# Kernel tuning notes

Measured on AMD Instinct MI355X. Metric: run time of the kernel, lower is better.

## Reference

```python
import jax, jax.numpy as jnp
import numpy as np

B, C, D, H, W = 2, 128, 32, 64, 64  # ch_in=128, shurink=0 -> Cs = ch_out = C
Cs = C


def setup_inputs() -> dict:
    key = jax.random.key(0)
    ks = jax.random.split(key, 9)
    std = 1.0 / np.sqrt(C).astype(np.float32)
    x = jax.random.normal(ks[0], (B, C, D, H, W), jnp.float32)
    Wk = jax.random.normal(ks[1], (Cs, C), jnp.float32) * std
    bk = jax.random.normal(ks[2], (Cs,), jnp.float32) * std
    Wq = jax.random.normal(ks[3], (Cs, C), jnp.float32) * std
    bq = jax.random.normal(ks[4], (Cs,), jnp.float32) * std
    Wv = jax.random.normal(ks[5], (Cs, C), jnp.float32) * std
    bv = jax.random.normal(ks[6], (Cs,), jnp.float32) * std
    Wo = jax.random.normal(ks[7], (C, Cs), jnp.float32) * (1.0 / np.sqrt(Cs).astype(np.float32))
    bo = jax.random.normal(ks[8], (C,), jnp.float32) * std
    return {"x": x, "Wk": Wk, "bk": bk, "Wq": Wq, "bq": bq, "Wv": Wv, "bv": bv, "Wo": Wo, "bo": bo}


def reference(x, Wk, bk, Wq, bq, Wv, bv, Wo, bo):
    # 1x1x1 Conv3d == per-voxel linear over channels
    def proj(Wt, bt):
        return jnp.einsum('bcdhw,oc->bodhw', x, Wt) + bt[None, :, None, None, None]

    K = proj(Wk, bk)  # [B,Cs,D,H,W]
    Q = proj(Wq, bq)
    V = proj(Wv, bv)

    scale = 1.0 / jnp.sqrt(jnp.asarray(Cs, x.dtype))
    # per-pixel depth attention: scores[b,h,w,i,j] = sum_c K[b,c,i,h,w] * Q[b,c,j,h,w]
    scores = jnp.einsum('bcihw,bcjhw->bhwij', K, Q) * scale
    # torch softmax dim=1 on [N,D,D] == key-position axis i (axis=-2 here)
    A = jax.nn.softmax(scores, axis=-2)
    # a[b,c,j,h,w] = sum_i V[b,c,i,h,w] * A[b,h,w,i,j]  (== bmm(V, A))
    a = jnp.einsum('bcihw,bhwij->bcjhw', V, A)
    out = jnp.einsum('bcjhw,oc->bojhw', a, Wo) + bo[None, :, None, None, None]
    return x + out  # atten_factor = 1
```

## Files before the change

### kernel.cpp

```cpp
#include <hip/hip_runtime.h>

typedef _Float16 f16x8 __attribute__((ext_vector_type(8)));
typedef _Float16 f16x4 __attribute__((ext_vector_type(4)));
typedef float    f32x4 __attribute__((ext_vector_type(4)));

#define MFMA(a,b,c) __builtin_amdgcn_mfma_f32_16x16x32_f16((a),(b),(c),0,0,0)


__global__ __launch_bounds__(128) void prep_kernel(
    const float* __restrict__ Wk, const float* __restrict__ bk,
    const float* __restrict__ Wq, const float* __restrict__ bq,
    const float* __restrict__ Wv, const float* __restrict__ bv,
    const float* __restrict__ Wo, const float* __restrict__ bo,
    _Float16* __restrict__ wh, float* __restrict__ bf) {
  __shared__ float worow[128];
  const int o = blockIdx.x;
  const int c = threadIdx.x;
  const float scale = 0.08838834764831844f;
  worow[c] = Wo[o*128 + c];
  __syncthreads();
  float acc = 0.f, a2 = 0.f;
  for (int m = 0; m < 128; ++m) {
    acc += worow[m] * Wv[m*128 + c];
    a2  += worow[m] * bv[m];
  }
  wh[o*128+c]         = (_Float16)(Wk[o*128+c] * scale);
  wh[16384 + o*128+c] = (_Float16)(Wq[o*128+c]);
  wh[32768 + o*128+c] = (_Float16)acc;
  if (c == 0) {
    bf[o]       = bk[o] * scale;
    bf[128 + o] = bq[o];
    bf[256 + o] = a2 + bo[o];
  }
}

__global__ __launch_bounds__(256) void transpose_kernel(
    const float* __restrict__ x, _Float16* __restrict__ Xg) {
  __shared__ _Float16 Lt[64 * 130];
  const int bid = blockIdx.x;
  const int h = bid & 63, d = (bid >> 6) & 31, b = bid >> 11;
  const int tid = threadIdx.x;
  const size_t rbase = (size_t)b*16777216u + (size_t)d*4096 + h*64;
#pragma unroll
  for (int i = 0; i < 8; ++i) {
    const int chunk = tid + i*256;
    const int c = chunk >> 4, wq = chunk & 15;
    const f32x4 v = *(const f32x4*)(x + rbase + (size_t)c*131072 + wq*4);
    Lt[(wq*4+0)*130 + c] = (_Float16)v[0];
    Lt[(wq*4+1)*130 + c] = (_Float16)v[1];
    Lt[(wq*4+2)*130 + c] = (_Float16)v[2];
    Lt[(wq*4+3)*130 + c] = (_Float16)v[3];
  }
  __syncthreads();
  const int gbase = b*1024 + h*16;
#pragma unroll
  for (int i = 0; i < 4; ++i) {
    const int idx = tid + i*256;
    const int w = idx >> 4, ck = (idx & 15) * 8;
    const int wg = w >> 2, p = w & 3;
    const f16x8 v = *(const f16x8*)(Lt + w*130 + ck);
    *(f16x8*)(Xg + (size_t)(gbase + wg)*16384 + (p*32 + d)*128 + ck) = v;
  }
}

__device__ __forceinline__ f16x4 cvt4(f32x4 v, f32x4 b) {
  f16x4 r;
  r[0] = (_Float16)(v[0] + b[0]); r[1] = (_Float16)(v[1] + b[1]);
  r[2] = (_Float16)(v[2] + b[2]); r[3] = (_Float16)(v[3] + b[3]);
  return r;
}
__device__ __forceinline__ f16x4 cvt4z(f32x4 v) {
  f16x4 r;
  r[0] = (_Float16)v[0]; r[1] = (_Float16)v[1];
  r[2] = (_Float16)v[2]; r[3] = (_Float16)v[3];
  return r;
}

__global__ __launch_bounds__(1024) void attn_kernel(
    const _Float16* __restrict__ Xg, const _Float16* __restrict__ wh,
    const float* __restrict__ bfp, float* __restrict__ out) {
  __shared__ __align__(16) char lds[133120];
  _Float16* Xt = (_Float16*)(lds);
  _Float16* Kt = (_Float16*)(lds + 34816);
  _Float16* Qt = (_Float16*)(lds + 69632);
  float*    Sm = (float*)(lds + 104448);
  _Float16* At = (_Float16*)(lds + 122880);
  float*    ot = (float*)(lds + 34816);

  const int tid  = threadIdx.x;
  const int lane = tid & 63;
  const int wv   = tid >> 6;
  const int quad = lane >> 4;
  const int l15  = lane & 15;
  const int mi   = wv & 7;
  const int ni   = wv >> 3;

  const int bid = blockIdx.x;
  const int g = (bid & ~31) | ((bid & 7) << 2) | ((bid >> 3) & 3);
  const int b   = g >> 10;
  const int rem = g & 1023;
  const int h   = rem >> 4;
  const int wg  = rem & 15;
  const size_t pbase = (size_t)b * 16777216u + (size_t)(h*64 + wg*4);

  f16x8 wk[4], wq[4], wp[4];
  {
    const int wrow = (mi*16 + l15) * 128;
#pragma unroll
    for (int kk = 0; kk < 4; ++kk) {
      const int off = wrow + kk*32 + quad*8;
      wk[kk] = *(const f16x8*)(wh + off);
      wq[kk] = *(const f16x8*)(wh + 16384 + off);
      wp[kk] = *(const f16x8*)(wh + 32768 + off);
    }
  }
  const f32x4 bk4 = *(const f32x4*)(bfp +       mi*16 + quad*4);
  const f32x4 bq4 = *(const f32x4*)(bfp + 128 + mi*16 + quad*4);
  const f32x4 bp4 = *(const f32x4*)(bfp + 256 + mi*16 + quad*4);
  const f32x4 zz = {0.f, 0.f, 0.f, 0.f};

  {
    const _Float16* src = Xg + (size_t)g * 16384;
#pragma unroll
    for (int i = 0; i < 2; ++i) {
      const int idx = tid + i*1024;
      const int row = idx >> 4, ck = (idx & 15) * 8;
      const f16x8 v = *(const f16x8*)(src + row*128 + ck);
      *(f16x8*)(Xt + row*136 + ck) = v;
    }
  }
  __syncthreads();

  {
    f32x4 aK[4] = {zz, zz, zz, zz};
    f32x4 aQ[4] = {zz, zz, zz, zz};
#pragma unroll
    for (int kk = 0; kk < 4; ++kk) {
      const int co = kk*32 + quad*8;
      f16x8 bfv[4];
#pragma unroll
      for (int nt = 0; nt < 4; ++nt)
        bfv[nt] = *(const f16x8*)(Xt + (ni*64 + nt*16 + l15)*136 + co);
#pragma unroll
      for (int nt = 0; nt < 4; ++nt) {
        aK[nt] = MFMA(wk[kk], bfv[nt], aK[nt]);
        aQ[nt] = MFMA(wq[kk], bfv[nt], aQ[nt]);
      }
    }
#pragma unroll
    for (int nt = 0; nt < 4; ++nt) {
      const int ad = (ni*64 + nt*16 + l15)*136 + mi*16 + quad*4;
      *(f16x4*)(Kt + ad) = cvt4(aK[nt], bk4);
      *(f16x4*)(Qt + ad) = cvt4(aQ[nt], bq4);
    }
  }
  __syncthreads();

  {
    const int p = wv >> 2, ti = (wv >> 1) & 1, tj = wv & 1;
    f32x4 aS = zz;
#pragma unroll
    for (int kk = 0; kk < 4; ++kk) {
      const int co = kk*32 + quad*8;
      const f16x8 ak  = *(const f16x8*)(Kt + (p*32 + ti*16 + l15)*136 + co);
      const f16x8 bq_ = *(const f16x8*)(Qt + (p*32 + tj*16 + l15)*136 + co);
      aS = MFMA(ak, bq_, aS);
    }
    *(f32x4*)(Sm + (p*32 + tj*16 + l15)*36 + ti*16 + quad*4) = aS;
  }
  __syncthreads();

  if (tid < 128) {
    const float* srow = Sm + tid*36;
    float mx = srow[0];
#pragma unroll
    for (int i = 1; i < 32; ++i) mx = fmaxf(mx, srow[i]);
    float den = 0.f;
#pragma unroll
    for (int i = 0; i < 32; ++i) den += __expf(srow[i] - mx);
    const float rr = 1.0f / den;
    _Float16* arow = At + tid*40;
#pragma unroll
    for (int i = 0; i < 32; ++i) arow[i] = (_Float16)(__expf(srow[i] - mx) * rr);
  }
  __syncthreads();

  {
    const int p = wv & 3, mg = wv >> 2;
    f16x8 bA[2];
#pragma unroll
    for (int tj = 0; tj < 2; ++tj)
      bA[tj] = *(const f16x8*)(At + (p*32 + tj*16 + l15)*40 + quad*8);
#pragma unroll
    for (int t2 = 0; t2 < 2; ++t2) {
      const int ms = mg*2 + t2;
      const int cbase = (p*32 + quad*8)*136 + ms*16 + l15;
      const f16x8 ax = { Xt[cbase], Xt[cbase+136], Xt[cbase+272], Xt[cbase+408],
                         Xt[cbase+544], Xt[cbase+680], Xt[cbase+816], Xt[cbase+952] };
#pragma unroll
      for (int tj = 0; tj < 2; ++tj) {
        f32x4 aU = MFMA(ax, bA[tj], zz);
        *(f16x4*)(Kt + (p*32 + tj*16 + l15)*136 + ms*16 + quad*4) = cvt4z(aU);
      }
    }
  }
  __syncthreads();

  f32x4 aO[4] = {zz, zz, zz, zz};
#pragma unroll
  for (int kk = 0; kk < 4; ++kk) {
    const int co = kk*32 + quad*8;
    f16x8 bfv[4];
#pragma unroll
    for (int nt = 0; nt < 4; ++nt)
      bfv[nt] = *(const f16x8*)(Kt + (ni*64 + nt*16 + l15)*136 + co);
#pragma unroll
    for (int nt = 0; nt < 4; ++nt)
      aO[nt] = MFMA(wp[kk], bfv[nt], aO[nt]);
  }
  __syncthreads();

#pragma unroll
  for (int nt = 0; nt < 4; ++nt) {
    const int col = ni*64 + nt*16 + l15;
    const int pp = col >> 5, jj = col & 31;
    float* dst = ot + (mi*16 + quad*4)*132 + jj*4 + pp;
    dst[0]   = aO[nt][0] + bp4[0];
    dst[132] = aO[nt][1] + bp4[1];
    dst[264] = aO[nt][2] + bp4[2];
    dst[396] = aO[nt][3] + bp4[3];
  }
  __syncthreads();

#pragma unroll
  for (int it = 0; it < 4; ++it) {
    const int o = it*32 + (tid >> 5);
    const int j = tid & 31;
    f32x4 v = *(const f32x4*)(ot + o*132 + j*4);
    v[0] += (float)Xt[(0*32 + j)*136 + o];
    v[1] += (float)Xt[(1*32 + j)*136 + o];
    v[2] += (float)Xt[(2*32 + j)*136 + o];
    v[3] += (float)Xt[(3*32 + j)*136 + o];
    *(f32x4*)(out + pbase + (size_t)o*131072 + j*4096) = v;
  }
}

extern "C" void kernel_launch(void* const* d_in, const int* in_sizes, int n_in,
                              void* d_out, int out_size, void* d_ws, size_t ws_size,
                              hipStream_t stream) {
  const float* x  = (const float*)d_in[0];
  const float* Wk = (const float*)d_in[1];
  const float* bk = (const float*)d_in[2];
  const float* Wq = (const float*)d_in[3];
  const float* bq = (const float*)d_in[4];
  const float* Wv = (const float*)d_in[5];
  const float* bv = (const float*)d_in[6];
  const float* Wo = (const float*)d_in[7];
  const float* bo = (const float*)d_in[8];
  float* out = (float*)d_out;
  _Float16* wh = (_Float16*)d_ws;
  float* bf = (float*)((char*)d_ws + 98304);
  _Float16* Xg = (_Float16*)((char*)d_ws + 131072);

  prep_kernel<<<dim3(128), dim3(128), 0, stream>>>(Wk, bk, Wq, bq, Wv, bv, Wo, bo, wh, bf);
  transpose_kernel<<<dim3(4096), dim3(256), 0, stream>>>(x, Xg);
  attn_kernel<<<dim3(2048), dim3(1024), 0, stream>>>(Xg, wh, bf, out);
}
```

Measured before the change: 378.7 us.

## Fold Wk·Wq into one projection, fuse transpose into attention kernel

Precomputes M = Wk^T·Wq (scaled) so scores become X^T·(M X + t), which removes one of the two projection GEMMs. The separate fp32-to-fp16 transpose kernel and its workspace round trip are dropped: the attention kernel now reads x directly into XOR-swizzled LDS. Softmax is computed in registers with wave shuffles, so the score staging buffer and one barrier go away. LDS usage drops, which could allow more resident blocks; the cost is uncoalesced strided global loads of x and possible fp16 precision loss from the folded weight product.

```diff
diff --git a/kernel.cpp b/kernel.cpp
--- a/kernel.cpp
+++ b/kernel.cpp
@@ -13,54 +13,23 @@
     const float* __restrict__ Wv, const float* __restrict__ bv,
     const float* __restrict__ Wo, const float* __restrict__ bo,
     _Float16* __restrict__ wh, float* __restrict__ bf) {
-  __shared__ float worow[128];
+  __shared__ float shK[128], shO[128];
   const int o = blockIdx.x;
   const int c = threadIdx.x;
   const float scale = 0.08838834764831844f;
-  worow[c] = Wo[o*128 + c];
-  __syncthreads();
-  float acc = 0.f, a2 = 0.f;
+  shK[c] = Wk[c*128 + o];
+  shO[c] = Wo[o*128 + c];
+  __syncthreads();
+  float aM = 0.f, aV = 0.f, tK = 0.f, bV = 0.f;
   for (int m = 0; m < 128; ++m) {
-    acc += worow[m] * Wv[m*128 + c];
-    a2  += worow[m] * bv[m];
-  }
-  wh[o*128+c]         = (_Float16)(Wk[o*128+c] * scale);
-  wh[16384 + o*128+c] = (_Float16)(Wq[o*128+c]);
-  wh[32768 + o*128+c] = (_Float16)acc;
-  if (c == 0) {
-    bf[o]       = bk[o] * scale;
-    bf[128 + o] = bq[o];
-    bf[256 + o] = a2 + bo[o];
-  }
-}
-
-__global__ __launch_bounds__(256) void transpose_kernel(
-    const float* __restrict__ x, _Float16* __restrict__ Xg) {
-  __shared__ _Float16 Lt[64 * 130];
-  const int bid = blockIdx.x;
-  const int h = bid & 63, d = (bid >> 6) & 31, b = bid >> 11;
-  const int tid = threadIdx.x;
-  const size_t rbase = (size_t)b*16777216u + (size_t)d*4096 + h*64;
-#pragma unroll
-  for (int i = 0; i < 8; ++i) {
-    const int chunk = tid + i*256;
-    const int c = chunk >> 4, wq = chunk & 15;
-    const f32x4 v = *(const f32x4*)(x + rbase + (size_t)c*131072 + wq*4);
-    Lt[(wq*4+0)*130 + c] = (_Float16)v[0];
-    Lt[(wq*4+1)*130 + c] = (_Float16)v[1];
-    Lt[(wq*4+2)*130 + c] = (_Float16)v[2];
-    Lt[(wq*4+3)*130 + c] = (_Float16)v[3];
-  }
-  __syncthreads();
-  const int gbase = b*1024 + h*16;
-#pragma unroll
-  for (int i = 0; i < 4; ++i) {
-    const int idx = tid + i*256;
-    const int w = idx >> 4, ck = (idx & 15) * 8;
-    const int wg = w >> 2, p = w & 3;
-    const f16x8 v = *(const f16x8*)(Lt + w*130 + ck);
-    *(f16x8*)(Xg + (size_t)(gbase + wg)*16384 + (p*32 + d)*128 + ck) = v;
-  }
+    aM += shK[m] * Wq[m*128 + c];
+    aV += shO[m] * Wv[m*128 + c];
+    tK += shK[m] * bq[m];
+    bV += shO[m] * bv[m];
+  }
+  wh[o*128 + c]         = (_Float16)(aM * scale);
+  wh[16384 + o*128 + c] = (_Float16)aV;
+  if (c == 0) { bf[o] = tK * scale; bf[128 + o] = bV + bo[o]; }
 }
 
 __device__ __forceinline__ f16x4 cvt4(f32x4 v, f32x4 b) {
@@ -76,24 +45,23 @@
   return r;
 }
 
-__global__ __launch_bounds__(1024) void attn_kernel(
-    const _Float16* __restrict__ Xg, const _Float16* __restrict__ wh,
+__device__ __forceinline__ int xsw(int row, int col ) {
+  return ((row << 8) | (col << 1)) ^ (((row ^ (row >> 2)) & 7) << 4);
+}
+
+__global__ __launch_bounds__(1024, 8) void attn_kernel(
+    const float* __restrict__ x, const _Float16* __restrict__ wh,
     const float* __restrict__ bfp, float* __restrict__ out) {
-  __shared__ __align__(16) char lds[133120];
-  _Float16* Xt = (_Float16*)(lds);
-  _Float16* Kt = (_Float16*)(lds + 34816);
-  _Float16* Qt = (_Float16*)(lds + 69632);
-  float*    Sm = (float*)(lds + 104448);
-  _Float16* At = (_Float16*)(lds + 122880);
-  float*    ot = (float*)(lds + 34816);
+  __shared__ __align__(16) char lds[75776];
+  char* XtB = lds;
+  char* YtB = lds + 32768;
+  _Float16* At = (_Float16*)(lds + 65536);
 
   const int tid  = threadIdx.x;
   const int lane = tid & 63;
   const int wv   = tid >> 6;
   const int quad = lane >> 4;
   const int l15  = lane & 15;
-  const int mi   = wv & 7;
-  const int ni   = wv >> 3;
 
   const int bid = blockIdx.x;
   const int g = (bid & ~31) | ((bid & 7) << 2) | ((bid >> 3) & 3);
@@ -102,90 +70,98 @@
   const int h   = rem >> 4;
   const int wg  = rem & 15;
   const size_t pbase = (size_t)b * 16777216u + (size_t)(h*64 + wg*4);
-
-  f16x8 wk[4], wq[4], wp[4];
-  {
-    const int wrow = (mi*16 + l15) * 128;
-#pragma unroll
-    for (int kk = 0; kk < 4; ++kk) {
-      const int off = wrow + kk*32 + quad*8;
-      wk[kk] = *(const f16x8*)(wh + off);
-      wq[kk] = *(const f16x8*)(wh + 16384 + off);
-      wp[kk] = *(const f16x8*)(wh + 32768 + off);
-    }
-  }
-  const f32x4 bk4 = *(const f32x4*)(bfp +       mi*16 + quad*4);
-  const f32x4 bq4 = *(const f32x4*)(bfp + 128 + mi*16 + quad*4);
-  const f32x4 bp4 = *(const f32x4*)(bfp + 256 + mi*16 + quad*4);
   const f32x4 zz = {0.f, 0.f, 0.f, 0.f};
 
-  {
-    const _Float16* src = Xg + (size_t)g * 16384;
-#pragma unroll
-    for (int i = 0; i < 2; ++i) {
+  const int mi = wv & 7, ni = wv >> 3;
+  f16x8 wm[4];
+#pragma unroll
+  for (int kk = 0; kk < 4; ++kk)
+    wm[kk] = *(const f16x8*)(wh + (mi*16 + l15)*128 + kk*32 + quad*8);
+  const f32x4 t4 = *(const f32x4*)(bfp + mi*16 + quad*4);
+
+  {
+    const float* xg = x + pbase;
+#pragma unroll
+    for (int i = 0; i < 4; ++i) {
       const int idx = tid + i*1024;
-      const int row = idx >> 4, ck = (idx & 15) * 8;
-      const f16x8 v = *(const f16x8*)(src + row*128 + ck);
-      *(f16x8*)(Xt + row*136 + ck) = v;
-    }
-  }
-  __syncthreads();
-
-  {
-    f32x4 aK[4] = {zz, zz, zz, zz};
-    f32x4 aQ[4] = {zz, zz, zz, zz};
+      const int c = idx & 127, dd = idx >> 7;
+      const f32x4 v = *(const f32x4*)(xg + (size_t)c*131072 + (size_t)dd*4096);
+#pragma unroll
+      for (int p = 0; p < 4; ++p)
+        *(_Float16*)(XtB + xsw(dd*4 + p, c)) = (_Float16)v[p];
+    }
+  }
+  __syncthreads();
+
+  {
+    f32x4 aY[4] = {zz, zz, zz, zz};
 #pragma unroll
     for (int kk = 0; kk < 4; ++kk) {
       const int co = kk*32 + quad*8;
-      f16x8 bfv[4];
-#pragma unroll
-      for (int nt = 0; nt < 4; ++nt)
-        bfv[nt] = *(const f16x8*)(Xt + (ni*64 + nt*16 + l15)*136 + co);
 #pragma unroll
       for (int nt = 0; nt < 4; ++nt) {
-        aK[nt] = MFMA(wk[kk], bfv[nt], aK[nt]);
-        aQ[nt] = MFMA(wq[kk], bfv[nt], aQ[nt]);
-      }
-    }
-#pragma unroll
-    for (int nt = 0; nt < 4; ++nt) {
-      const int ad = (ni*64 + nt*16 + l15)*136 + mi*16 + quad*4;
-      *(f16x4*)(Kt + ad) = cvt4(aK[nt], bk4);
-      *(f16x4*)(Qt + ad) = cvt4(aQ[nt], bq4);
-    }
-  }
-  __syncthreads();
-
-  {
-    const int p = wv >> 2, ti = (wv >> 1) & 1, tj = wv & 1;
-    f32x4 aS = zz;
+        const f16x8 bfv = *(const f16x8*)(XtB + xsw(ni*64 + nt*16 + l15, co));
+        aY[nt] = MFMA(wm[kk], bfv, aY[nt]);
+      }
+    }
+#pragma unroll
+    for (int nt = 0; nt < 4; ++nt)
+      *(f16x4*)(YtB + xsw(ni*64 + nt*16 + l15, mi*16 + quad*4)) = cvt4(aY[nt], t4);
+  }
+  __syncthreads();
+
+  if (wv < 4) {
+    const int p = wv;
+    f32x4 aS[2][2] = {{zz, zz}, {zz, zz}};
 #pragma unroll
     for (int kk = 0; kk < 4; ++kk) {
       const int co = kk*32 + quad*8;
-      const f16x8 ak  = *(const f16x8*)(Kt + (p*32 + ti*16 + l15)*136 + co);
-      const f16x8 bq_ = *(const f16x8*)(Qt + (p*32 + tj*16 + l15)*136 + co);
-      aS = MFMA(ak, bq_, aS);
-    }
-    *(f32x4*)(Sm + (p*32 + tj*16 + l15)*36 + ti*16 + quad*4) = aS;
-  }
-  __syncthreads();
-
-  if (tid < 128) {
-    const float* srow = Sm + tid*36;
-    float mx = srow[0];
-#pragma unroll
-    for (int i = 1; i < 32; ++i) mx = fmaxf(mx, srow[i]);
-    float den = 0.f;
-#pragma unroll
-    for (int i = 0; i < 32; ++i) den += __expf(srow[i] - mx);
-    const float rr = 1.0f / den;
-    _Float16* arow = At + tid*40;
-#pragma unroll
-    for (int i = 0; i < 32; ++i) arow[i] = (_Float16)(__expf(srow[i] - mx) * rr);
-  }
-  __syncthreads();
-
-  {
+      f16x8 ak[2], by[2];
+#pragma unroll
+      for (int t = 0; t < 2; ++t) {
+        ak[t] = *(const f16x8*)(XtB + xsw((t*16 + l15)*4 + p, co));
+        by[t] = *(const f16x8*)(YtB + xsw((t*16 + l15)*4 + p, co));
+      }
+#pragma unroll
+      for (int ti = 0; ti < 2; ++ti)
+#pragma unroll
+        for (int tj = 0; tj < 2; ++tj)
+          aS[ti][tj] = MFMA(ak[ti], by[tj], aS[ti][tj]);
+    }
+#pragma unroll
+    for (int tj = 0; tj < 2; ++tj) {
+      float mx = aS[0][tj][0];
+#pragma unroll
+      for (int r = 1; r < 4; ++r) mx = fmaxf(mx, aS[0][tj][r]);
+#pragma unroll
+      for (int r = 0; r < 4; ++r) mx = fmaxf(mx, aS[1][tj][r]);
+      mx = fmaxf(mx, __shfl_xor(mx, 16));
+      mx = fmaxf(mx, __shfl_xor(mx, 32));
+      float e[2][4];
+      float den = 0.f;
+#pragma unroll
+      for (int ti = 0; ti < 2; ++ti)
+#pragma unroll
+        for (int r = 0; r < 4; ++r) { e[ti][r] = __expf(aS[ti][tj][r] - mx); den += e[ti][r]; }
+      den += __shfl_xor(den, 16);
+      den += __shfl_xor(den, 32);
+      const float rr = 1.0f / den;
+#pragma unroll
+      for (int ti = 0; ti < 2; ++ti) {
+        f16x4 av;
+#pragma unroll
+        for (int r = 0; r < 4; ++r) av[r] = (_Float16)(e[ti][r] * rr);
+        *(f16x4*)(At + (p*32 + tj*16 + l15)*40 + ti*16 + quad*4) = av;
+      }
+    }
+  }
+  __syncthreads();
+
+  f16x8 wp[4];
+  {
+#pragma unroll
+    for (int kk = 0; kk < 4; ++kk)
+      wp[kk] = *(const f16x8*)(wh + 16384 + ((wv & 7)*16 + l15)*128 + kk*32 + quad*8);
     const int p = wv & 3, mg = wv >> 2;
     f16x8 bA[2];
 #pragma unroll
@@ -194,54 +170,45 @@
 #pragma unroll
     for (int t2 = 0; t2 < 2; ++t2) {
       const int ms = mg*2 + t2;
-      const int cbase = (p*32 + quad*8)*136 + ms*16 + l15;
-      const f16x8 ax = { Xt[cbase], Xt[cbase+136], Xt[cbase+272], Xt[cbase+408],
-                         Xt[cbase+544], Xt[cbase+680], Xt[cbase+816], Xt[cbase+952] };
+      f16x8 ax;
+#pragma unroll
+      for (int jj = 0; jj < 8; ++jj)
+        ax[jj] = *(const _Float16*)(XtB + xsw((quad*8 + jj)*4 + p, ms*16 + l15));
 #pragma unroll
       for (int tj = 0; tj < 2; ++tj) {
-        f32x4 aU = MFMA(ax, bA[tj], zz);
-        *(f16x4*)(Kt + (p*32 + tj*16 + l15)*136 + ms*16 + quad*4) = cvt4z(aU);
-      }
-    }
-  }
-  __syncthreads();
-
-  f32x4 aO[4] = {zz, zz, zz, zz};
-#pragma unroll
-  for (int kk = 0; kk < 4; ++kk) {
-    const int co = kk*32 + quad*8;
-    f16x8 bfv[4];
-#pragma unroll
-    for (int nt = 0; nt < 4; ++nt)
-      bfv[nt] = *(const f16x8*)(Kt + (ni*64 + nt*16 + l15)*136 + co);
-#pragma unroll
-    for (int nt = 0; nt < 4; ++nt)
-      aO[nt] = MFMA(wp[kk], bfv[nt], aO[nt]);
-  }
-  __syncthreads();
-
-#pragma unroll
-  for (int nt = 0; nt < 4; ++nt) {
-    const int col = ni*64 + nt*16 + l15;
-    const int pp = col >> 5, jj = col & 31;
-    float* dst = ot + (mi*16 + quad*4)*132 + jj*4 + pp;
-    dst[0]   = aO[nt][0] + bp4[0];
-    dst[132] = aO[nt][1] + bp4[1];
-    dst[264] = aO[nt][2] + bp4[2];
-    dst[396] = aO[nt][3] + bp4[3];
-  }
-  __syncthreads();
-
-#pragma unroll
-  for (int it = 0; it < 4; ++it) {
-    const int o = it*32 + (tid >> 5);
-    const int j = tid & 31;
-    f32x4 v = *(const f32x4*)(ot + o*132 + j*4);
-    v[0] += (float)Xt[(0*32 + j)*136 + o];
-    v[1] += (float)Xt[(1*32 + j)*136 + o];
-    v[2] += (float)Xt[(2*32 + j)*136 + o];
-    v[3] += (float)Xt[(3*32 + j)*136 + o];
-    *(f32x4*)(out + pbase + (size_t)o*131072 + j*4096) = v;
+        const f32x4 aU = MFMA(ax, bA[tj], zz);
+        *(f16x4*)(YtB + xsw((tj*16 + l15)*4 + p, ms*16 + quad*4)) = cvt4z(aU);
+      }
+    }
+  }
+  __syncthreads();
+
+  {
+    const int oi = wv & 7, mg6 = wv >> 3;
+    f32x4 acc[4] = {zz, zz, zz, zz};
+#pragma unroll
+    for (int kk = 0; kk < 4; ++kk) {
+      const int co = kk*32 + quad*8;
+#pragma unroll
+      for (int mt = 0; mt < 4; ++mt) {
+        const f16x8 av = *(const f16x8*)(YtB + xsw((mg6*4 + mt)*16 + l15, co));
+        acc[mt] = MFMA(av, wp[kk], acc[mt]);
+      }
+    }
+    const int o = oi*16 + l15;
+    const float bb = bfp[128 + o];
+    float* outp = out + pbase + (size_t)o*131072;
+#pragma unroll
+    for (int mt = 0; mt < 4; ++mt) {
+      const int colb = (mg6*4 + mt)*16 + quad*4;
+      const int d = colb >> 2;
+      f32x4 v;
+#pragma unroll
+      for (int r = 0; r < 4; ++r)
+        v[r] = acc[mt][r] + bb +
+               (float)*(const _Float16*)(XtB + xsw(colb + r, o));
+      *(f32x4*)(outp + (size_t)d*4096) = v;
+    }
   }
 }
 
@@ -259,10 +226,8 @@
   const float* bo = (const float*)d_in[8];
   float* out = (float*)d_out;
   _Float16* wh = (_Float16*)d_ws;
-  float* bf = (float*)((char*)d_ws + 98304);
-  _Float16* Xg = (_Float16*)((char*)d_ws + 131072);
+  float* bf = (float*)((char*)d_ws + 65536);
 
   prep_kernel<<<dim3(128), dim3(128), 0, stream>>>(Wk, bk, Wq, bq, Wv, bv, Wo, bo, wh, bf);
-  transpose_kernel<<<dim3(4096), dim3(256), 0, stream>>>(x, Xg);
-  attn_kernel<<<dim3(2048), dim3(1024), 0, stream>>>(Xg, wh, bf, out);
-}
+  attn_kernel<<<dim3(2048), dim3(1024), 0, stream>>>(x, wh, bf, out);
+}
```

Result: slower. 386.4 us (+2.0%).
